# Optimization experiments

Measured on AMD Instinct MI355X. Metric: run time of the kernel, lower is better.

## Reference

```python
import jax, jax.numpy as jnp
import numpy as np


def setup_inputs() -> dict:
    key = jax.random.key(0)
    k1, k2, k3, k4 = jax.random.split(key, 4)
    N, E, D, F = 100000, 1600000, 128, 128
    features = jax.random.normal(k1, (N, D), dtype=jnp.float32)
    W = jax.random.normal(k2, (D, F), dtype=jnp.float32) * (1.0 / np.sqrt(D))
    b = jnp.zeros((F,), dtype=jnp.float32)
    edge_src = jax.random.randint(k3, (E,), 0, N, dtype=jnp.int32)
    edge_dst = jax.random.randint(k4, (E,), 0, N, dtype=jnp.int32)
    return {"features": features, "W": W, "b": b,
            "edge_src": edge_src, "edge_dst": edge_dst}


def reference(features, W, b, edge_src, edge_dst):
    # GCN message passing: copy_src -> sum reduce (SpMM with unit weights)
    N = features.shape[0]
    msgs = features[edge_src]                                  # [E, D] gather
    h = jax.ops.segment_sum(msgs, edge_dst, num_segments=N)    # [N, D] scatter-add
    # Linear(out_feats) + relu activation (no batch_norm, no dropout)
    out = jax.nn.relu(h @ W + b)                               # [N, F]
    return out
```

## Files before the change

### kernel.cpp

```cpp
#include <hip/hip_runtime.h>


constexpr int D     = 128;
constexpr int F     = 128;
constexpr int NCH   = 192;
constexpr int CAPC  = 16;
constexpr int NBF   = 1600;
constexpr int OVCAP = 16384;
constexpr int LCAP  = 120;

typedef short bf16x8 __attribute__((ext_vector_type(8)));
typedef float f32x4  __attribute__((ext_vector_type(4)));

__device__ __forceinline__ unsigned bf16_rne(float f) {
  unsigned u = __float_as_uint(f);
  return (u + 0x7FFFu + ((u >> 16) & 1u)) >> 16;
}

__global__ __launch_bounds__(256) void wsplit_kernel(
    const float* __restrict__ W,
    unsigned short* __restrict__ Wht,
    unsigned short* __restrict__ Wlt,
    int* __restrict__ ovf_cnt) {
  int i = blockIdx.x * 256 + threadIdx.x;
  if (i == 0) *ovf_cnt = 0;
  int k = i >> 7;
  int c = i & 127;
  float w = W[i];
  unsigned h = bf16_rne(w);
  float hf = __uint_as_float(h << 16);
  unsigned l = bf16_rne(w - hf);
  Wht[c * 128 + k] = (unsigned short)h;
  Wlt[c * 128 + k] = (unsigned short)l;
}

__global__ __launch_bounds__(1024) void megaprep_kernel(
    const int* __restrict__ src,
    const int* __restrict__ dst,
    int* __restrict__ gcnt,
    int* __restrict__ gslot,
    int* __restrict__ ovf_cnt,
    int2* __restrict__ ovf,
    const float* __restrict__ X,
    const unsigned short* __restrict__ Wht,
    const unsigned short* __restrict__ Wlt,
    uint2* __restrict__ Y,
    int E, int NB, int CH, int N) {
  __shared__ __align__(16) char smem[NBF * 16 * 4 + NBF * 4];
  int bid = blockIdx.x;
  int tid = threadIdx.x;

  if (bid < NCH) {
    int* cells = (int*)smem;
    int* lcnt  = (int*)(smem + NBF * 16 * 4);
    int c = bid;
    for (int i = tid; i < NB; i += 1024) lcnt[i] = 0;
    __syncthreads();

    int e0 = c * CH;
    int e1 = min(E, e0 + CH);
    for (int e = e0 + tid; e < e1; e += 1024) {
      int t = dst[e];
      int s = src[e];
      int bucket = t >> 6;
      int entry = s | ((t & 63) << 17);
      int pos = atomicAdd(&lcnt[bucket], 1);
      if (pos < CAPC) {
        cells[bucket * CAPC + pos] = entry;
      } else {
        int gp = atomicAdd(ovf_cnt, 1);
        if (gp < OVCAP) ovf[gp] = make_int2(entry, bucket);
      }
    }
    __syncthreads();

    {
      int nb4 = (NB * CAPC) >> 2;
      int4* g4 = (int4*)(gslot + (size_t)c * NB * CAPC);
      const int4* c4p = (const int4*)cells;
      for (int i = tid; i < nb4; i += 1024) g4[i] = c4p[i];
    }
    for (int i = tid; i < NB; i += 1024)
      gcnt[(size_t)c * NB + i] = lcnt[i];
    return;
  }

  float* cst = (float*)smem;
  int lane = tid & 63;
  int wv = tid >> 6;
  int r = lane & 15;
  int g = lane >> 4;
  int unit = bid - NCH;
  int rowbase = unit * 256;
  int row = rowbase + wv * 16 + r;
  const float* xrow = X + (size_t)min(row, N - 1) * 128;

  f32x4 acc[8];
#pragma unroll
  for (int ct = 0; ct < 8; ++ct) acc[ct] = (f32x4){0.f, 0.f, 0.f, 0.f};

#pragma unroll
  for (int ks = 0; ks < 4; ++ks) {
    int k0 = ks * 32 + g * 8;
    float xf[8];
    *(float4*)&xf[0] = *(const float4*)(xrow + k0);
    *(float4*)&xf[4] = *(const float4*)(xrow + k0 + 4);
    union { bf16x8 v; unsigned u4[4]; } ahi, alo;
#pragma unroll
    for (int p = 0; p < 4; ++p) {
      unsigned h0 = bf16_rne(xf[2 * p]);
      unsigned h1 = bf16_rne(xf[2 * p + 1]);
      float f0 = __uint_as_float(h0 << 16);
      float f1 = __uint_as_float(h1 << 16);
      unsigned l0 = bf16_rne(xf[2 * p] - f0);
      unsigned l1 = bf16_rne(xf[2 * p + 1] - f1);
      ahi.u4[p] = h0 | (h1 << 16);
      alo.u4[p] = l0 | (l1 << 16);
    }
#pragma unroll
    for (int ct = 0; ct < 8; ++ct) {
      size_t bo = (size_t)(ct * 16 + r) * 128 + k0;
      bf16x8 bh = *(const bf16x8*)(Wht + bo);
      bf16x8 bl = *(const bf16x8*)(Wlt + bo);
      acc[ct] = __builtin_amdgcn_mfma_f32_16x16x32_bf16(ahi.v, bh, acc[ct], 0, 0, 0);
      acc[ct] = __builtin_amdgcn_mfma_f32_16x16x32_bf16(alo.v, bh, acc[ct], 0, 0, 0);
      acc[ct] = __builtin_amdgcn_mfma_f32_16x16x32_bf16(ahi.v, bl, acc[ct], 0, 0, 0);
    }
  }

#pragma unroll
  for (int h = 0; h < 4; ++h) {
    if ((wv >> 2) == h) {
      int lwv = wv & 3;
#pragma unroll
      for (int ct = 0; ct < 8; ++ct) {
        int col = ct * 16 + r;
#pragma unroll
        for (int v = 0; v < 4; ++v)
          cst[(lwv * 16 + g * 4 + v) * 132 + col] = acc[ct][v];
      }
    }
    __syncthreads();
    int c4 = tid & 31;
#pragma unroll
    for (int it = 0; it < 2; ++it) {
      int i = it * 1024 + tid;
      int rl = i >> 5;
      int orow = rowbase + h * 64 + rl;
      if (orow < N) {
        float4 cv = *(const float4*)&cst[rl * 132 + c4 * 4];
        uint2 o;
        o.x = bf16_rne(cv.x) | (bf16_rne(cv.y) << 16);
        o.y = bf16_rne(cv.z) | (bf16_rne(cv.w) << 16);
        Y[(size_t)orow * 32 + c4] = o;
      }
    }
    __syncthreads();
  }
}

__global__ __launch_bounds__(256) void accum_kernel(
    const uint2* __restrict__ yb,
    const int* __restrict__ gcnt,
    const int* __restrict__ gslot,
    const int* __restrict__ ovf_cnt,
    const int2* __restrict__ ovf,
    const float* __restrict__ b,
    float* __restrict__ out,
    int N, int NB) {
  __shared__ float hl[64 * 64];
  __shared__ int ccnt[NCH];
  __shared__ int lists[16 * LCAP];
  __shared__ int lcount[16];

  int bid = blockIdx.x;
  int bb = bid >> 1;
  int fh = bid & 1;
  int tid = threadIdx.x;
  float4* hl4 = (float4*)hl;

  float4 z4 = make_float4(0.f, 0.f, 0.f, 0.f);
#pragma unroll
  for (int i = 0; i < 4; ++i) hl4[i * 256 + tid] = z4;
  if (tid < NCH) ccnt[tid] = min(gcnt[(size_t)tid * NB + bb], CAPC);
  if (tid < 16) lcount[tid] = 0;
  __syncthreads();

  for (int i0 = 0; i0 < NCH * CAPC; i0 += 256) {
    int i = i0 + tid;
    int c = i >> 4;
    int slot = i & (CAPC - 1);
    int entry = gslot[((size_t)c * NB + bb) * CAPC + slot];
    if (slot < ccnt[c]) {
      int o = (entry >> 17) & 15;
      int pos = atomicAdd(&lcount[o], 1);
      if (pos < LCAP) lists[o * LCAP + pos] = entry;
    }
  }
  __syncthreads();

  int l = tid & 15;
  int g = tid >> 4;
  int n = min(lcount[g], LCAP);
  const int* Lg = &lists[g * LCAP];
  const uint2* ybh = yb + fh * 16;

  int j = 0;
  for (; j + 16 <= n; j += 16) {
    uint2 v[16];
    int en[16];
#pragma unroll
    for (int k = 0; k < 16; ++k) {
      en[k] = Lg[j + k];
      v[k] = ybh[(size_t)(en[k] & 0x1FFFF) * 32 + l];
    }
#pragma unroll
    for (int k = 0; k < 16; ++k) {
      int dl = (en[k] >> 17) & 63;
      float4 h = hl4[dl * 16 + l];
      h.x += __uint_as_float(v[k].x << 16);
      h.y += __uint_as_float(v[k].x & 0xFFFF0000u);
      h.z += __uint_as_float(v[k].y << 16);
      h.w += __uint_as_float(v[k].y & 0xFFFF0000u);
      hl4[dl * 16 + l] = h;
    }
  }
  for (; j + 4 <= n; j += 4) {
    uint2 v[4];
    int en[4];
#pragma unroll
    for (int k = 0; k < 4; ++k) {
      en[k] = Lg[j + k];
      v[k] = ybh[(size_t)(en[k] & 0x1FFFF) * 32 + l];
    }
#pragma unroll
    for (int k = 0; k < 4; ++k) {
      int dl = (en[k] >> 17) & 63;
      float4 h = hl4[dl * 16 + l];
      h.x += __uint_as_float(v[k].x << 16);
      h.y += __uint_as_float(v[k].x & 0xFFFF0000u);
      h.z += __uint_as_float(v[k].y << 16);
      h.w += __uint_as_float(v[k].y & 0xFFFF0000u);
      hl4[dl * 16 + l] = h;
    }
  }
  for (; j < n; ++j) {
    int e = Lg[j];
    uint2 v = ybh[(size_t)(e & 0x1FFFF) * 32 + l];
    int dl = (e >> 17) & 63;
    float4 h = hl4[dl * 16 + l];
    h.x += __uint_as_float(v.x << 16);
    h.y += __uint_as_float(v.x & 0xFFFF0000u);
    h.z += __uint_as_float(v.y << 16);
    h.w += __uint_as_float(v.y & 0xFFFF0000u);
    hl4[dl * 16 + l] = h;
  }

  __syncthreads();
  int nov = min(*ovf_cnt, OVCAP);
  if (nov > 0) {
    int2* ovbuf = (int2*)lists;
    for (int base = 0; base < nov; base += 800) {
      int m = min(nov - base, 800);
      for (int i = tid; i < m; i += 256) ovbuf[i] = ovf[base + i];
      __syncthreads();
      for (int i = 0; i < m; ++i) {
        int2 oe = ovbuf[i];
        if (oe.y == bb && (((oe.x >> 17) & 15) == g)) {
          uint2 v = ybh[(size_t)(oe.x & 0x1FFFF) * 32 + l];
          int dl = (oe.x >> 17) & 63;
          float4 h = hl4[dl * 16 + l];
          h.x += __uint_as_float(v.x << 16);
          h.y += __uint_as_float(v.x & 0xFFFF0000u);
          h.z += __uint_as_float(v.y << 16);
          h.w += __uint_as_float(v.y & 0xFFFF0000u);
          hl4[dl * 16 + l] = h;
        }
      }
      __syncthreads();
    }
  }
  __syncthreads();

  int c4 = tid & 15;
  float4 bv = ((const float4*)b)[fh * 16 + c4];
  int row0 = bb * 64;
#pragma unroll
  for (int it = 0; it < 4; ++it) {
    int i = it * 256 + tid;
    int rl = i >> 4;
    int row = row0 + rl;
    if (row < N) {
      float4 h = hl4[rl * 16 + c4];
      float4 o;
      o.x = fmaxf(h.x + bv.x, 0.f);
      o.y = fmaxf(h.y + bv.y, 0.f);
      o.z = fmaxf(h.z + bv.z, 0.f);
      o.w = fmaxf(h.w + bv.w, 0.f);
      ((float4*)out)[(size_t)row * (F / 4) + fh * 16 + c4] = o;
    }
  }
}

extern "C" void kernel_launch(void* const* d_in, const int* in_sizes, int n_in,
                              void* d_out, int out_size, void* d_ws, size_t ws_size,
                              hipStream_t stream) {
  const float* feat = (const float*)d_in[0];
  const float* W    = (const float*)d_in[1];
  const float* bv   = (const float*)d_in[2];
  const int* src    = (const int*)d_in[3];
  const int* dst    = (const int*)d_in[4];

  int N = in_sizes[0] / D;
  int E = in_sizes[3];

  int NB = (N + 63) / 64;
  int CH = (E + NCH - 1) / NCH;
  int NU = (N + 255) / 256;

  uint2* yb     = (uint2*)d_ws;
  int* gcnt     = (int*)((char*)d_ws + (26u << 20));
  int* ovf_cnt  = (int*)((char*)d_ws + (28u << 20));
  int2* ovf     = (int2*)((char*)d_ws + (28u << 20) + 256);
  int* gslot    = (int*)((char*)d_ws + (29u << 20));
  unsigned short* Wht = (unsigned short*)((char*)d_ws + (50u << 20));
  unsigned short* Wlt = Wht + 128 * 128;

  float* out = (float*)d_out;

  wsplit_kernel<<<64, 256, 0, stream>>>(W, Wht, Wlt, ovf_cnt);

  megaprep_kernel<<<NCH + NU, 1024, 0, stream>>>(
      src, dst, gcnt, gslot, ovf_cnt, ovf, feat, Wht, Wlt, yb, E, NB, CH, N);

  accum_kernel<<<2 * NB, 256, 0, stream>>>(yb, gcnt, gslot, ovf_cnt, ovf,
                                           bv, out, N, NB);
}
```

Before: 243.5 us.

## Split edge bucketing blocks into four destination-range quarters to shrink LDS

Each edge-chunk bucketing block is replaced by four blocks, each handling only destinations in one quarter of the node range (512 buckets). This cuts the shared-memory footprint per block from about 106KB to about 34KB, so more blocks can be resident per CU and the GEMM blocks sharing the kernel also get more occupancy. The cost is that every quarter block rereads the full src/dst chunk, which quadruples edge-index reads.

```diff
diff --git a/kernel.cpp b/kernel.cpp
--- a/kernel.cpp
+++ b/kernel.cpp
@@ -5,7 +5,7 @@
 constexpr int F     = 128;
 constexpr int NCH   = 192;
 constexpr int CAPC  = 16;
-constexpr int NBF   = 1600;
+constexpr int NBQ   = 512;
 constexpr int OVCAP = 16384;
 constexpr int LCAP  = 120;
 
@@ -46,15 +46,16 @@
     const unsigned short* __restrict__ Wlt,
     uint2* __restrict__ Y,
     int E, int NB, int CH, int N) {
-  __shared__ __align__(16) char smem[NBF * 16 * 4 + NBF * 4];
+  __shared__ __align__(16) char smem[NBQ * 16 * 4 + NBQ * 4];
   int bid = blockIdx.x;
   int tid = threadIdx.x;
 
-  if (bid < NCH) {
+  if (bid < 4 * NCH) {
     int* cells = (int*)smem;
-    int* lcnt  = (int*)(smem + NBF * 16 * 4);
-    int c = bid;
-    for (int i = tid; i < NB; i += 1024) lcnt[i] = 0;
+    int* lcnt  = (int*)(smem + NBQ * 16 * 4);
+    int c = bid >> 2;
+    int q = bid & 3;
+    for (int i = tid; i < NBQ; i += 1024) lcnt[i] = 0;
     __syncthreads();
 
     int e0 = c * CH;
@@ -62,26 +63,30 @@
     for (int e = e0 + tid; e < e1; e += 1024) {
       int t = dst[e];
       int s = src[e];
-      int bucket = t >> 6;
-      int entry = s | ((t & 63) << 17);
-      int pos = atomicAdd(&lcnt[bucket], 1);
-      if (pos < CAPC) {
-        cells[bucket * CAPC + pos] = entry;
-      } else {
-        int gp = atomicAdd(ovf_cnt, 1);
-        if (gp < OVCAP) ovf[gp] = make_int2(entry, bucket);
+      if ((t >> 15) == q) {
+        int local = (t >> 6) & (NBQ - 1);
+        int entry = s | ((t & 63) << 17);
+        int pos = atomicAdd(&lcnt[local], 1);
+        if (pos < CAPC) {
+          cells[local * CAPC + pos] = entry;
+        } else {
+          int gp = atomicAdd(ovf_cnt, 1);
+          if (gp < OVCAP) ovf[gp] = make_int2(entry, t >> 6);
+        }
       }
     }
     __syncthreads();
 
-    {
-      int nb4 = (NB * CAPC) >> 2;
-      int4* g4 = (int4*)(gslot + (size_t)c * NB * CAPC);
+    int qlo = q * NBQ;
+    int qn = min(NB - qlo, NBQ);
+    if (qn > 0) {
+      int nb4 = (qn * CAPC) >> 2;
+      int4* g4 = (int4*)(gslot + ((size_t)c * NB + qlo) * CAPC);
       const int4* c4p = (const int4*)cells;
       for (int i = tid; i < nb4; i += 1024) g4[i] = c4p[i];
-    }
-    for (int i = tid; i < NB; i += 1024)
-      gcnt[(size_t)c * NB + i] = lcnt[i];
+      for (int i = tid; i < qn; i += 1024)
+        gcnt[(size_t)c * NB + qlo + i] = lcnt[i];
+    }
     return;
   }
 
@@ -90,7 +95,7 @@
   int wv = tid >> 6;
   int r = lane & 15;
   int g = lane >> 4;
-  int unit = bid - NCH;
+  int unit = bid - 4 * NCH;
   int rowbase = unit * 256;
   int row = rowbase + wv * 16 + r;
   const float* xrow = X + (size_t)min(row, N - 1) * 128;
@@ -330,7 +335,7 @@
 
   wsplit_kernel<<<64, 256, 0, stream>>>(W, Wht, Wlt, ovf_cnt);
 
-  megaprep_kernel<<<NCH + NU, 1024, 0, stream>>>(
+  megaprep_kernel<<<4 * NCH + NU, 1024, 0, stream>>>(
       src, dst, gcnt, gslot, ovf_cnt, ovf, feat, Wht, Wlt, yb, E, NB, CH, N);
 
   accum_kernel<<<2 * NB, 256, 0, stream>>>(yb, gcnt, gslot, ovf_cnt, ovf,
```

Result: slower. 257.5 us (+5.8%).

## Fuse W bf16 split into megaprep and stage split weights in LDS

Applied to the files above, without the earlier changes.

Drops the separate weight-split kernel. Each GEMM block of the prep kernel now converts W into hi/lo bf16 halves itself, stores them in shared memory with a padded stride, and its MFMA loop reads B fragments from LDS instead of global memory. The overflow counter reset moves to a hipMemsetAsync. This removes one launch and the global round trip for the split weights, but every one of about 391 GEMM blocks now repeats the 64 KB read and conversion of W plus an extra barrier before its main work.

```diff
diff --git a/kernel.cpp b/kernel.cpp
--- a/kernel.cpp
+++ b/kernel.cpp
@@ -8,6 +8,7 @@
 constexpr int NBF   = 1600;
 constexpr int OVCAP = 16384;
 constexpr int LCAP  = 120;
+constexpr int WSTR  = 136;
 
 typedef short bf16x8 __attribute__((ext_vector_type(8)));
 typedef float f32x4  __attribute__((ext_vector_type(4)));
@@ -15,23 +16,6 @@
 __device__ __forceinline__ unsigned bf16_rne(float f) {
   unsigned u = __float_as_uint(f);
   return (u + 0x7FFFu + ((u >> 16) & 1u)) >> 16;
-}
-
-__global__ __launch_bounds__(256) void wsplit_kernel(
-    const float* __restrict__ W,
-    unsigned short* __restrict__ Wht,
-    unsigned short* __restrict__ Wlt,
-    int* __restrict__ ovf_cnt) {
-  int i = blockIdx.x * 256 + threadIdx.x;
-  if (i == 0) *ovf_cnt = 0;
-  int k = i >> 7;
-  int c = i & 127;
-  float w = W[i];
-  unsigned h = bf16_rne(w);
-  float hf = __uint_as_float(h << 16);
-  unsigned l = bf16_rne(w - hf);
-  Wht[c * 128 + k] = (unsigned short)h;
-  Wlt[c * 128 + k] = (unsigned short)l;
 }
 
 __global__ __launch_bounds__(1024) void megaprep_kernel(
@@ -42,8 +26,7 @@
     int* __restrict__ ovf_cnt,
     int2* __restrict__ ovf,
     const float* __restrict__ X,
-    const unsigned short* __restrict__ Wht,
-    const unsigned short* __restrict__ Wlt,
+    const float* __restrict__ W,
     uint2* __restrict__ Y,
     int E, int NB, int CH, int N) {
   __shared__ __align__(16) char smem[NBF * 16 * 4 + NBF * 4];
@@ -85,7 +68,22 @@
     return;
   }
 
-  float* cst = (float*)smem;
+  unsigned short* whi = (unsigned short*)smem;
+  unsigned short* wlo = (unsigned short*)(smem + 34816);
+  float* cst = (float*)(smem + 69632);
+
+  for (int i = tid; i < 128 * 128; i += 1024) {
+    int k = i >> 7;
+    int c = i & 127;
+    float w = W[i];
+    unsigned h = bf16_rne(w);
+    float hf = __uint_as_float(h << 16);
+    unsigned lo = bf16_rne(w - hf);
+    whi[c * WSTR + k] = (unsigned short)h;
+    wlo[c * WSTR + k] = (unsigned short)lo;
+  }
+  __syncthreads();
+
   int lane = tid & 63;
   int wv = tid >> 6;
   int r = lane & 15;
@@ -119,9 +117,9 @@
     }
 #pragma unroll
     for (int ct = 0; ct < 8; ++ct) {
-      size_t bo = (size_t)(ct * 16 + r) * 128 + k0;
-      bf16x8 bh = *(const bf16x8*)(Wht + bo);
-      bf16x8 bl = *(const bf16x8*)(Wlt + bo);
+      int bo = (ct * 16 + r) * WSTR + k0;
+      bf16x8 bh = *(const bf16x8*)(whi + bo);
+      bf16x8 bl = *(const bf16x8*)(wlo + bo);
       acc[ct] = __builtin_amdgcn_mfma_f32_16x16x32_bf16(ahi.v, bh, acc[ct], 0, 0, 0);
       acc[ct] = __builtin_amdgcn_mfma_f32_16x16x32_bf16(alo.v, bh, acc[ct], 0, 0, 0);
       acc[ct] = __builtin_amdgcn_mfma_f32_16x16x32_bf16(ahi.v, bl, acc[ct], 0, 0, 0);
@@ -130,6 +128,7 @@
 
 #pragma unroll
   for (int h = 0; h < 4; ++h) {
+    __syncthreads();
     if ((wv >> 2) == h) {
       int lwv = wv & 3;
 #pragma unroll
@@ -155,7 +154,6 @@
         Y[(size_t)orow * 32 + c4] = o;
       }
     }
-    __syncthreads();
   }
 }
 
@@ -323,15 +321,13 @@
   int* ovf_cnt  = (int*)((char*)d_ws + (28u << 20));
   int2* ovf     = (int2*)((char*)d_ws + (28u << 20) + 256);
   int* gslot    = (int*)((char*)d_ws + (29u << 20));
-  unsigned short* Wht = (unsigned short*)((char*)d_ws + (50u << 20));
-  unsigned short* Wlt = Wht + 128 * 128;
 
   float* out = (float*)d_out;
 
-  wsplit_kernel<<<64, 256, 0, stream>>>(W, Wht, Wlt, ovf_cnt);
+  hipMemsetAsync(ovf_cnt, 0, sizeof(int), stream);
 
   megaprep_kernel<<<NCH + NU, 1024, 0, stream>>>(
-      src, dst, gcnt, gslot, ovf_cnt, ovf, feat, Wht, Wlt, yb, E, NB, CH, N);
+      src, dst, gcnt, gslot, ovf_cnt, ovf, feat, W, yb, E, NB, CH, N);
 
   accum_kernel<<<2 * NB, 256, 0, stream>>>(yb, gcnt, gslot, ovf_cnt, ovf,
                                            bv, out, N, NB);
```

New measurement: 197.2 us. 1.23x faster.
